# Kernel tuning notes

Hardware: AMD Instinct MI355X
Metric: run time of the kernel (lower is better)

The kernel has to match this reference:

```python
import jax, jax.numpy as jnp
import numpy as np

B, N, M = 2, 4096, 4096
QUERY_DIM, CONTEXT_DIM = 512, 768
H, D = 8, 64
INNER = H * D


def setup_inputs() -> dict:
    key = jax.random.key(0)
    ks = jax.random.split(key, 8)
    x = jax.random.normal(ks[0], (B, N, QUERY_DIM), dtype=jnp.float32)
    context_tensor = jax.random.normal(ks[1], (B, M, CONTEXT_DIM), dtype=jnp.float32)
    mask = jax.random.randint(ks[2], (B, M), 0, 2) > 0  # bool [B, M]
    s = 0.02
    Wq = jax.random.normal(ks[3], (QUERY_DIM, INNER), dtype=jnp.float32) * s
    Wk = jax.random.normal(ks[4], (CONTEXT_DIM, INNER), dtype=jnp.float32) * s
    Wv = jax.random.normal(ks[5], (CONTEXT_DIM, INNER), dtype=jnp.float32) * s
    Wo = jax.random.normal(ks[6], (INNER, QUERY_DIM), dtype=jnp.float32) * s
    bo = jnp.zeros((QUERY_DIM,), dtype=jnp.float32)
    return {"x": x, "context_tensor": context_tensor, "mask": mask,
            "Wq": Wq, "Wk": Wk, "Wv": Wv, "Wo": Wo, "bo": bo}


def reference(x, context_tensor, mask, Wq, Wk, Wv, Wo, bo):
    scale = D ** (-0.5)
    # projections -> [B, T, H, D]
    q = (x @ Wq).reshape(B, N, H, D)
    k = (context_tensor @ Wk).reshape(B, M, H, D)
    v = (context_tensor @ Wv).reshape(B, M, H, D)
    # scores [B, H, N, M]
    attn = jnp.einsum('bnhd,bmhd->bhnm', q, k) * scale
    neg = -jnp.finfo(attn.dtype).max
    attn = jnp.where(mask[:, None, None, :], attn, neg)
    attn = jax.nn.softmax(attn, axis=-1)
    out = jnp.einsum('bhnm,bmhd->bnhd', attn, v).reshape(B, N, INNER)
    return out @ Wo + bo  # dropout is 0.0 -> identity
```

## Files before the change

### kernel.cpp

```cpp
#include <hip/hip_runtime.h>

typedef unsigned short u16;
typedef unsigned int u32;
typedef __attribute__((ext_vector_type(8))) short bf16x8;
typedef __attribute__((ext_vector_type(4))) short bf16x4;
typedef __attribute__((ext_vector_type(4))) float f32x4;

#define CSC 0.1803368801111244f

__device__ __forceinline__ u16 f2b(float f) {
  union { float f; u32 u; } c; c.f = f;
  return (u16)((c.u + 0x8000u) >> 16);
}

__device__ __forceinline__ uint2 pk4(f32x4 p) {
  union { float f; u32 u; } c0, c1, c2, c3;
  c0.f = p[0]; c1.f = p[1]; c2.f = p[2]; c3.f = p[3];
  u32 a = c0.u + 0x8000u, b = c1.u + 0x8000u;
  u32 c = c2.u + 0x8000u, d = c3.u + 0x8000u;
  uint2 r;
  r.x = __builtin_amdgcn_perm(b, a, 0x07060302u);
  r.y = __builtin_amdgcn_perm(d, c, 0x07060302u);
  return r;
}

__device__ __forceinline__ bf16x4 pk4v(f32x4 p) {
  union { uint2 u; bf16x4 v; } c;
  c.u = pk4(p);
  return c.v;
}

__device__ __forceinline__ void async16(const void* g, void* s) {
  __builtin_amdgcn_global_load_lds(
      (const __attribute__((address_space(1))) u32*)g,
      (__attribute__((address_space(3))) u32*)s, 16, 0, 0);
}

__global__ void prep(const float* __restrict__ x, const float* __restrict__ ctx,
                     const int* __restrict__ mask,
                     const float* __restrict__ Wq, const float* __restrict__ Wk,
                     const float* __restrict__ Wv, const float* __restrict__ Wo,
                     u16* __restrict__ Xb, u16* __restrict__ Cb, float* __restrict__ mbf,
                     u16* __restrict__ Wtq, u16* __restrict__ Wtkv, u16* __restrict__ Wto) {
  __shared__ u16 Tl[64 * 65];
  const int bid = blockIdx.x, tid = threadIdx.x;
  if (bid < 10240) {
    const float* src; u16* dst; int i;
    if (bid < 4096) { i = (bid * 256 + tid) * 4; src = x; dst = Xb; }
    else { i = ((bid - 4096) * 256 + tid) * 4; src = ctx; dst = Cb; }
    float4 f = *(const float4*)&src[i];
    ushort4 o;
    o.x = f2b(f.x); o.y = f2b(f.y); o.z = f2b(f.z); o.w = f2b(f.w);
    *(ushort4*)&dst[i] = o;
  } else if (bid < 10560) {
    int t = bid - 10240;
    const float* W; u16* Wt; int Kd, tt;
    if (t < 64)       { W = Wq; Wt = Wtq;  Kd = 512; tt = t; }
    else if (t < 160) { W = Wk; Wt = Wtkv; Kd = 768; tt = t - 64; }
    else if (t < 256) { W = Wv; Wt = Wtkv + (size_t)512 * 768; Kd = 768; tt = t - 160; }
    else              { W = Wo; Wt = Wto;  Kd = 512; tt = t - 256; }
    const int k0 = (tt >> 3) * 64, n0 = (tt & 7) * 64;
    {
      const int r = tid >> 2, cg = (tid & 3) * 16;
#pragma unroll
      for (int i = 0; i < 4; i++) {
        float4 f = *(const float4*)&W[(size_t)(k0 + r) * 512 + n0 + cg + i * 4];
        Tl[r * 65 + cg + i * 4 + 0] = f2b(f.x);
        Tl[r * 65 + cg + i * 4 + 1] = f2b(f.y);
        Tl[r * 65 + cg + i * 4 + 2] = f2b(f.z);
        Tl[r * 65 + cg + i * 4 + 3] = f2b(f.w);
      }
    }
    __syncthreads();
    {
      const int n = tid >> 2, kg = (tid & 3) * 16;
      u16 buf[16];
#pragma unroll
      for (int i = 0; i < 16; i++) buf[i] = Tl[(kg + i) * 65 + n];
      u16* dst = &Wt[(size_t)(n0 + n) * Kd + k0 + kg];
      *(uint4*)dst = *(const uint4*)&buf[0];
      *(uint4*)(dst + 8) = *(const uint4*)&buf[8];
    }
  } else {
    int i = (bid - 10560) * 256 + tid;
    mbf[i] = mask[i] ? 0.f : -1e30f;
  }
}

__global__ __launch_bounds__(256, 2)
void gemm_qkv(const u16* __restrict__ Xb, const u16* __restrict__ Cb,
              const u16* __restrict__ Wtq, const u16* __restrict__ Wtkv,
              u16* __restrict__ Qb, u16* __restrict__ Kb, u16* __restrict__ Vt) {
  __shared__ u16 As[128 * 64];
  __shared__ u16 Bs[128 * 64];
  const int tid = threadIdx.x;
  const int w = tid >> 6, lane = tid & 63, quad = lane >> 4, l16 = lane & 15;
  const int wr = w >> 1, wc = w & 1;
  const int y = blockIdx.y;
  const bool isQ = (y < 4);
  const u16* A  = isQ ? Xb : Cb;
  const u16* Bt = isQ ? Wtq : Wtkv;
  const int K   = isQ ? 512 : 768;
  const int n0  = isQ ? y * 128 : (y - 4) * 128;
  const size_t m0 = (size_t)blockIdx.x * 128;
  const u16* Ab = A + m0 * K;
  const u16* Bb = Bt + (size_t)n0 * K;

  const int cswz = (((lane & 7) ^ ((lane >> 3) & 7)) << 3);
  const int sw0 = ((quad ^ (l16 & 7)) << 3);
  const int sw1 = sw0 ^ 32;
  const int rA = w * 32 + (lane >> 3);

  f32x4 acc[4][4];
#pragma unroll
  for (int i = 0; i < 4; i++)
#pragma unroll
    for (int j = 0; j < 4; j++) acc[i][j] = (f32x4){0.f, 0.f, 0.f, 0.f};

  for (int k0 = 0; k0 < K; k0 += 64) {
#pragma unroll
    for (int t = 0; t < 4; t++) {
      async16(Ab + (size_t)(rA + t * 8) * K + k0 + cswz, &As[(w * 32 + t * 8) * 64]);
      async16(Bb + (size_t)(rA + t * 8) * K + k0 + cswz, &Bs[(w * 32 + t * 8) * 64]);
    }
    __syncthreads();
#pragma unroll
    for (int ks = 0; ks < 2; ks++) {
      const int so = ks ? sw1 : sw0;
      bf16x8 af[4], bfr[4];
#pragma unroll
      for (int i = 0; i < 4; i++) {
        af[i]  = *(const bf16x8*)&As[(wr * 64 + i * 16 + l16) * 64 + so];
        bfr[i] = *(const bf16x8*)&Bs[(wc * 64 + i * 16 + l16) * 64 + so];
      }
#pragma unroll
      for (int i = 0; i < 4; i++)
#pragma unroll
        for (int j = 0; j < 4; j++)
          acc[i][j] = __builtin_amdgcn_mfma_f32_16x16x32_bf16(af[i], bfr[j], acc[i][j], 0, 0, 0);
    }
    __syncthreads();
  }

  if (!isQ && n0 >= 512) {
#pragma unroll
    for (int i = 0; i < 4; i++)
#pragma unroll
      for (int j = 0; j < 4; j++) {
        size_t row0 = m0 + wr * 64 + i * 16 + quad * 4;
        int d = n0 - 512 + wc * 64 + j * 16 + l16;
        *(uint2*)&Vt[(size_t)d * 8192 + row0] = pk4(acc[i][j]);
      }
  } else {
    u16* C0 = isQ ? Qb : Kb;
#pragma unroll
    for (int i = 0; i < 4; i++)
#pragma unroll
      for (int j = 0; j < 4; j++)
#pragma unroll
        for (int r = 0; r < 4; r++) {
          size_t row = m0 + wr * 64 + i * 16 + quad * 4 + r;
          int col = n0 + wc * 64 + j * 16 + l16;
          C0[row * 512 + col] = f2b(acc[i][j][r]);
        }
  }
}

__global__ __launch_bounds__(256, 2)
void gemm_o(const u16* __restrict__ A, const u16* __restrict__ Bt,
            const float* __restrict__ bias, float* __restrict__ Cf) {
  __shared__ u16 As[64 * 64];
  __shared__ u16 Bs[128 * 64];
  const int tid = threadIdx.x;
  const int w = tid >> 6, lane = tid & 63, quad = lane >> 4, l16 = lane & 15;
  const int wr = w >> 1, wc = w & 1;
  const size_t m0 = (size_t)blockIdx.x * 64;
  const int n0 = blockIdx.y * 128;
  const u16* Ab = A + m0 * 512;
  const u16* Bb = Bt + (size_t)n0 * 512;

  const int cswz = (((lane & 7) ^ ((lane >> 3) & 7)) << 3);
  const int sw0 = ((quad ^ (l16 & 7)) << 3);
  const int sw1 = sw0 ^ 32;
  const int r8 = lane >> 3;

  f32x4 acc[2][4];
#pragma unroll
  for (int i = 0; i < 2; i++)
#pragma unroll
    for (int j = 0; j < 4; j++) acc[i][j] = (f32x4){0.f, 0.f, 0.f, 0.f};

  for (int k0 = 0; k0 < 512; k0 += 64) {
#pragma unroll
    for (int t = 0; t < 2; t++)
      async16(Ab + (size_t)(w * 16 + t * 8 + r8) * 512 + k0 + cswz, &As[(w * 16 + t * 8) * 64]);
#pragma unroll
    for (int t = 0; t < 4; t++)
      async16(Bb + (size_t)(w * 32 + t * 8 + r8) * 512 + k0 + cswz, &Bs[(w * 32 + t * 8) * 64]);
    __syncthreads();
#pragma unroll
    for (int ks = 0; ks < 2; ks++) {
      const int so = ks ? sw1 : sw0;
      bf16x8 af[2], bfr[4];
#pragma unroll
      for (int i = 0; i < 2; i++)
        af[i] = *(const bf16x8*)&As[(wr * 32 + i * 16 + l16) * 64 + so];
#pragma unroll
      for (int j = 0; j < 4; j++)
        bfr[j] = *(const bf16x8*)&Bs[(wc * 64 + j * 16 + l16) * 64 + so];
#pragma unroll
      for (int i = 0; i < 2; i++)
#pragma unroll
        for (int j = 0; j < 4; j++)
          acc[i][j] = __builtin_amdgcn_mfma_f32_16x16x32_bf16(af[i], bfr[j], acc[i][j], 0, 0, 0);
    }
    __syncthreads();
  }

#pragma unroll
  for (int i = 0; i < 2; i++)
#pragma unroll
    for (int j = 0; j < 4; j++)
#pragma unroll
      for (int r = 0; r < 4; r++) {
        size_t row = m0 + wr * 32 + i * 16 + quad * 4 + r;
        int col = n0 + wc * 64 + j * 16 + l16;
        Cf[row * 512 + col] = acc[i][j][r] + bias[col];
      }
}

__global__ __launch_bounds__(256, 2)
void attn_kernel(const u16* __restrict__ Q, const u16* __restrict__ Kg,
                 const u16* __restrict__ Vt, const float* __restrict__ mbf,
                 u16* __restrict__ AO) {
  __shared__ u16 Ks[2][64 * 64];
  __shared__ u16 Vs[2][64 * 64];
  __shared__ float Mf[4096];

  const int tid = threadIdx.x;
  const int w = tid >> 6, lane = tid & 63, quad = lane >> 4, l16 = lane & 15;
  const int l = blockIdx.x;
  const int qb = l >> 4, hb = l & 15, h = hb >> 1, b = hb & 1;
  const size_t qrow0 = (size_t)b * 4096 + (size_t)qb * 128;
  const size_t crow0 = (size_t)b * 4096;
  const int hcol = h * 64;

  const int cswz = (((lane & 7) ^ ((lane >> 3) & 7)) << 3);
  const int sw0 = ((quad ^ (l16 & 7)) << 3);
  const int sw1 = sw0 ^ 32;
  const int r8 = lane >> 3;

  bf16x8 qf[2][2];
#pragma unroll
  for (int qt = 0; qt < 2; qt++)
#pragma unroll
    for (int ks = 0; ks < 2; ks++)
      qf[qt][ks] = *(const bf16x8*)&Q[(qrow0 + w * 32 + qt * 16 + l16) * 512 + hcol + ks * 32 + quad * 8];

  async16(Kg + (crow0 + w * 16 + r8) * 512 + hcol + cswz, &Ks[0][(w * 16) * 64]);
  async16(Kg + (crow0 + w * 16 + 8 + r8) * 512 + hcol + cswz, &Ks[0][(w * 16 + 8) * 64]);
  async16(Vt + (size_t)(hcol + w * 16 + r8) * 8192 + crow0 + cswz, &Vs[0][(w * 16) * 64]);
  async16(Vt + (size_t)(hcol + w * 16 + 8 + r8) * 8192 + crow0 + cswz, &Vs[0][(w * 16 + 8) * 64]);
#pragma unroll
  for (int t = 0; t < 4; t++) {
    int i = w * 4 + t;
    async16(mbf + crow0 + i * 256 + lane * 4, &Mf[i * 256]);
  }
  __syncthreads();

  f32x4 Oacc[2][4];
#pragma unroll
  for (int qt = 0; qt < 2; qt++)
#pragma unroll
    for (int dt = 0; dt < 4; dt++) Oacc[qt][dt] = (f32x4){0.f, 0.f, 0.f, 0.f};
  float lsum[2] = {0.f, 0.f};

  for (int mt = 0; mt < 64; mt++) {
    const int cur = mt & 1;
    const size_t m0 = (size_t)mt * 64;

    if (mt < 63) {
      const size_t mn = m0 + 64;
      async16(Kg + (crow0 + mn + w * 16 + r8) * 512 + hcol + cswz, &Ks[cur ^ 1][(w * 16) * 64]);
      async16(Kg + (crow0 + mn + w * 16 + 8 + r8) * 512 + hcol + cswz, &Ks[cur ^ 1][(w * 16 + 8) * 64]);
      async16(Vt + (size_t)(hcol + w * 16 + r8) * 8192 + crow0 + mn + cswz, &Vs[cur ^ 1][(w * 16) * 64]);
      async16(Vt + (size_t)(hcol + w * 16 + 8 + r8) * 8192 + crow0 + mn + cswz, &Vs[cur ^ 1][(w * 16 + 8) * 64]);
    }

    f32x4 mv[4];
#pragma unroll
    for (int mtt = 0; mtt < 4; mtt++)
      mv[mtt] = *(const f32x4*)&Mf[m0 + mtt * 16 + quad * 4];

    f32x4 sacc[2][4];
#pragma unroll
    for (int qt = 0; qt < 2; qt++)
#pragma unroll
      for (int mtt = 0; mtt < 4; mtt++) sacc[qt][mtt] = (f32x4){0.f, 0.f, 0.f, 0.f};
#pragma unroll
    for (int ks = 0; ks < 2; ks++) {
      const int so = ks ? sw1 : sw0;
      bf16x8 kb[4];
#pragma unroll
      for (int mtt = 0; mtt < 4; mtt++)
        kb[mtt] = *(const bf16x8*)&Ks[cur][(mtt * 16 + l16) * 64 + so];
#pragma unroll
      for (int qt = 0; qt < 2; qt++)
#pragma unroll
        for (int mtt = 0; mtt < 4; mtt++)
          sacc[qt][mtt] = __builtin_amdgcn_mfma_f32_16x16x32_bf16(kb[mtt], qf[qt][ks], sacc[qt][mtt], 0, 0, 0);
    }

    bf16x4 pf[2][4];
#pragma unroll
    for (int qt = 0; qt < 2; qt++) {
      float rs = 0.f;
#pragma unroll
      for (int mtt = 0; mtt < 4; mtt++) {
        f32x4 p;
#pragma unroll
        for (int r = 0; r < 4; r++) {
          p[r] = __builtin_amdgcn_exp2f(fmaf(sacc[qt][mtt][r], CSC, mv[mtt][r]));
          rs += p[r];
        }
        pf[qt][mtt] = pk4v(p);
      }
      lsum[qt] += rs;
    }

#pragma unroll
    for (int mtt = 0; mtt < 4; mtt++) {
      bf16x4 va[4];
#pragma unroll
      for (int dt = 0; dt < 4; dt++)
        va[dt] = *(const bf16x4*)&Vs[cur][(dt * 16 + l16) * 64 +
                    (((mtt * 2 + (quad >> 1)) ^ (l16 & 7)) << 3) + ((quad & 1) << 2)];
#pragma unroll
      for (int qt = 0; qt < 2; qt++)
#pragma unroll
        for (int dt = 0; dt < 4; dt++)
          Oacc[qt][dt] = __builtin_amdgcn_mfma_f32_16x16x16bf16_1k(va[dt], pf[qt][mtt], Oacc[qt][dt], 0, 0, 0);
    }
    __syncthreads();
  }

  float inv[2];
#pragma unroll
  for (int qt = 0; qt < 2; qt++) {
    float lv = lsum[qt];
    lv += __shfl_xor(lv, 16);
    lv += __shfl_xor(lv, 32);
    inv[qt] = 1.0f / lv;
  }

#pragma unroll
  for (int qt = 0; qt < 2; qt++)
#pragma unroll
    for (int dt = 0; dt < 4; dt++) {
      f32x4 o;
#pragma unroll
      for (int r = 0; r < 4; r++) o[r] = Oacc[qt][dt][r] * inv[qt];
      *(uint2*)&AO[(qrow0 + w * 32 + qt * 16 + l16) * 512 + hcol + dt * 16 + quad * 4] = pk4(o);
    }
}


extern "C" void kernel_launch(void* const* d_in, const int* in_sizes, int n_in,
                              void* d_out, int out_size, void* d_ws, size_t ws_size,
                              hipStream_t stream) {
  const float* x   = (const float*)d_in[0];
  const float* ctx = (const float*)d_in[1];
  const int*  mask = (const int*)d_in[2];
  const float* Wq  = (const float*)d_in[3];
  const float* Wk  = (const float*)d_in[4];
  const float* Wv  = (const float*)d_in[5];
  const float* Wo  = (const float*)d_in[6];
  const float* bo  = (const float*)d_in[7];
  float* out = (float*)d_out;

  char* p = (char*)d_ws;
  u16* Xb   = (u16*)p; p += (size_t)8192 * 512 * 2;
  u16* Cb   = (u16*)p; p += (size_t)8192 * 768 * 2;
  u16* Wtq  = (u16*)p; p += (size_t)512 * 512 * 2;
  u16* Wtkv = (u16*)p; p += (size_t)1024 * 768 * 2;
  u16* Wto  = (u16*)p; p += (size_t)512 * 512 * 2;
  u16* Qb   = (u16*)p; p += (size_t)8192 * 512 * 2;
  u16* Kb   = (u16*)p; p += (size_t)8192 * 512 * 2;
  u16* Vtg  = (u16*)p; p += (size_t)512 * 8192 * 2;
  u16* AOb  = (u16*)p; p += (size_t)8192 * 512 * 2;
  float* mbf = (float*)p; p += (size_t)8192 * 4;

  prep<<<10592, 256, 0, stream>>>(x, ctx, mask, Wq, Wk, Wv, Wo,
                                  Xb, Cb, mbf, Wtq, Wtkv, Wto);
  gemm_qkv<<<dim3(64, 12), 256, 0, stream>>>(Xb, Cb, Wtq, Wtkv, Qb, Kb, Vtg);
  attn_kernel<<<512, 256, 0, stream>>>(Qb, Kb, Vtg, mbf, AOb);
  gemm_o<<<dim3(128, 4), 256, 0, stream>>>(AOb, Wto, bo, out);
}
```

Before: 240.9 us.

## Fold key mask and softmax scale into K/V projections and shrink tiles

The projection GEMM now multiplies K rows by the mask and the softmax scale, and multiplies V rows by the mask. Masked keys therefore give a zero score, so exp2 yields exactly 1 and a zero V contribution. The attention kernel drops the per-tile mask loads and the FMA before exp2, then corrects the row sum by subtracting the per-batch count of masked keys, which prep computes. All three GEMM and attention kernels move to smaller tiles (64-row blocks), with more blocks and higher launch-bound occupancy targets. The trade-off is less K/V reuse per attention block and more global traffic in exchange for more parallelism and fewer instructions per tile.

```diff
diff --git a/kernel.cpp b/kernel.cpp
--- a/kernel.cpp
+++ b/kernel.cpp
@@ -40,9 +40,11 @@
                      const int* __restrict__ mask,
                      const float* __restrict__ Wq, const float* __restrict__ Wk,
                      const float* __restrict__ Wv, const float* __restrict__ Wo,
-                     u16* __restrict__ Xb, u16* __restrict__ Cb, float* __restrict__ mbf,
+                     u16* __restrict__ Xb, u16* __restrict__ Cb,
+                     float* __restrict__ mvalid, float* __restrict__ cnt,
                      u16* __restrict__ Wtq, u16* __restrict__ Wtkv, u16* __restrict__ Wto) {
   __shared__ u16 Tl[64 * 65];
+  __shared__ int cred[4];
   const int bid = blockIdx.x, tid = threadIdx.x;
   if (bid < 10240) {
     const float* src; u16* dst; int i;
@@ -82,16 +84,31 @@
       *(uint4*)(dst + 8) = *(const uint4*)&buf[8];
     }
   } else {
-    int i = (bid - 10560) * 256 + tid;
-    mbf[i] = mask[i] ? 0.f : -1e30f;
-  }
-}
-
-__global__ __launch_bounds__(256, 2)
+    const int b = bid - 10560;
+    const int base = b * 4096;
+    const int w = tid >> 6, lane = tid & 63;
+    int zc = 0;
+#pragma unroll
+    for (int j = 0; j < 16; j++) {
+      int idx = tid + j * 256;
+      int mv = mask[base + idx];
+      mvalid[base + idx] = mv ? 1.f : 0.f;
+      zc += (mv == 0);
+    }
+#pragma unroll
+    for (int d = 1; d < 64; d <<= 1) zc += __shfl_xor(zc, d);
+    if (lane == 0) cred[w] = zc;
+    __syncthreads();
+    if (tid == 0) cnt[b] = (float)(cred[0] + cred[1] + cred[2] + cred[3]);
+  }
+}
+
+__global__ __launch_bounds__(256, 6)
 void gemm_qkv(const u16* __restrict__ Xb, const u16* __restrict__ Cb,
               const u16* __restrict__ Wtq, const u16* __restrict__ Wtkv,
+              const float* __restrict__ mvalid,
               u16* __restrict__ Qb, u16* __restrict__ Kb, u16* __restrict__ Vt) {
-  __shared__ u16 As[128 * 64];
+  __shared__ u16 As[64 * 64];
   __shared__ u16 Bs[128 * 64];
   const int tid = threadIdx.x;
   const int w = tid >> 6, lane = tid & 63, quad = lane >> 4, l16 = lane & 15;
@@ -102,82 +119,9 @@
   const u16* Bt = isQ ? Wtq : Wtkv;
   const int K   = isQ ? 512 : 768;
   const int n0  = isQ ? y * 128 : (y - 4) * 128;
-  const size_t m0 = (size_t)blockIdx.x * 128;
+  const size_t m0 = (size_t)blockIdx.x * 64;
   const u16* Ab = A + m0 * K;
   const u16* Bb = Bt + (size_t)n0 * K;
-
-  const int cswz = (((lane & 7) ^ ((lane >> 3) & 7)) << 3);
-  const int sw0 = ((quad ^ (l16 & 7)) << 3);
-  const int sw1 = sw0 ^ 32;
-  const int rA = w * 32 + (lane >> 3);
-
-  f32x4 acc[4][4];
-#pragma unroll
-  for (int i = 0; i < 4; i++)
-#pragma unroll
-    for (int j = 0; j < 4; j++) acc[i][j] = (f32x4){0.f, 0.f, 0.f, 0.f};
-
-  for (int k0 = 0; k0 < K; k0 += 64) {
-#pragma unroll
-    for (int t = 0; t < 4; t++) {
-      async16(Ab + (size_t)(rA + t * 8) * K + k0 + cswz, &As[(w * 32 + t * 8) * 64]);
-      async16(Bb + (size_t)(rA + t * 8) * K + k0 + cswz, &Bs[(w * 32 + t * 8) * 64]);
-    }
-    __syncthreads();
-#pragma unroll
-    for (int ks = 0; ks < 2; ks++) {
-      const int so = ks ? sw1 : sw0;
-      bf16x8 af[4], bfr[4];
-#pragma unroll
-      for (int i = 0; i < 4; i++) {
-        af[i]  = *(const bf16x8*)&As[(wr * 64 + i * 16 + l16) * 64 + so];
-        bfr[i] = *(const bf16x8*)&Bs[(wc * 64 + i * 16 + l16) * 64 + so];
-      }
-#pragma unroll
-      for (int i = 0; i < 4; i++)
-#pragma unroll
-        for (int j = 0; j < 4; j++)
-          acc[i][j] = __builtin_amdgcn_mfma_f32_16x16x32_bf16(af[i], bfr[j], acc[i][j], 0, 0, 0);
-    }
-    __syncthreads();
-  }
-
-  if (!isQ && n0 >= 512) {
-#pragma unroll
-    for (int i = 0; i < 4; i++)
-#pragma unroll
-      for (int j = 0; j < 4; j++) {
-        size_t row0 = m0 + wr * 64 + i * 16 + quad * 4;
-        int d = n0 - 512 + wc * 64 + j * 16 + l16;
-        *(uint2*)&Vt[(size_t)d * 8192 + row0] = pk4(acc[i][j]);
-      }
-  } else {
-    u16* C0 = isQ ? Qb : Kb;
-#pragma unroll
-    for (int i = 0; i < 4; i++)
-#pragma unroll
-      for (int j = 0; j < 4; j++)
-#pragma unroll
-        for (int r = 0; r < 4; r++) {
-          size_t row = m0 + wr * 64 + i * 16 + quad * 4 + r;
-          int col = n0 + wc * 64 + j * 16 + l16;
-          C0[row * 512 + col] = f2b(acc[i][j][r]);
-        }
-  }
-}
-
-__global__ __launch_bounds__(256, 2)
-void gemm_o(const u16* __restrict__ A, const u16* __restrict__ Bt,
-            const float* __restrict__ bias, float* __restrict__ Cf) {
-  __shared__ u16 As[64 * 64];
-  __shared__ u16 Bs[128 * 64];
-  const int tid = threadIdx.x;
-  const int w = tid >> 6, lane = tid & 63, quad = lane >> 4, l16 = lane & 15;
-  const int wr = w >> 1, wc = w & 1;
-  const size_t m0 = (size_t)blockIdx.x * 64;
-  const int n0 = blockIdx.y * 128;
-  const u16* Ab = A + m0 * 512;
-  const u16* Bb = Bt + (size_t)n0 * 512;
 
   const int cswz = (((lane & 7) ^ ((lane >> 3) & 7)) << 3);
   const int sw0 = ((quad ^ (l16 & 7)) << 3);
@@ -190,13 +134,12 @@
 #pragma unroll
     for (int j = 0; j < 4; j++) acc[i][j] = (f32x4){0.f, 0.f, 0.f, 0.f};
 
-  for (int k0 = 0; k0 < 512; k0 += 64) {
-#pragma unroll
-    for (int t = 0; t < 2; t++)
-      async16(Ab + (size_t)(w * 16 + t * 8 + r8) * 512 + k0 + cswz, &As[(w * 16 + t * 8) * 64]);
+  for (int k0 = 0; k0 < K; k0 += 64) {
+    async16(Ab + (size_t)(w * 16 + r8) * K + k0 + cswz, &As[(w * 16) * 64]);
+    async16(Ab + (size_t)(w * 16 + 8 + r8) * K + k0 + cswz, &As[(w * 16 + 8) * 64]);
 #pragma unroll
     for (int t = 0; t < 4; t++)
-      async16(Bb + (size_t)(w * 32 + t * 8 + r8) * 512 + k0 + cswz, &Bs[(w * 32 + t * 8) * 64]);
+      async16(Bb + (size_t)(w * 32 + t * 8 + r8) * K + k0 + cswz, &Bs[(w * 32 + t * 8) * 64]);
     __syncthreads();
 #pragma unroll
     for (int ks = 0; ks < 2; ks++) {
@@ -217,63 +160,130 @@
     __syncthreads();
   }
 
-#pragma unroll
-  for (int i = 0; i < 2; i++)
-#pragma unroll
-    for (int j = 0; j < 4; j++)
-#pragma unroll
-      for (int r = 0; r < 4; r++) {
-        size_t row = m0 + wr * 32 + i * 16 + quad * 4 + r;
-        int col = n0 + wc * 64 + j * 16 + l16;
-        Cf[row * 512 + col] = acc[i][j][r] + bias[col];
-      }
-}
-
-__global__ __launch_bounds__(256, 2)
+  if (isQ) {
+#pragma unroll
+    for (int i = 0; i < 2; i++)
+#pragma unroll
+      for (int j = 0; j < 4; j++)
+#pragma unroll
+        for (int r = 0; r < 4; r++) {
+          size_t row = m0 + wr * 32 + i * 16 + quad * 4 + r;
+          Qb[row * 512 + n0 + wc * 64 + j * 16 + l16] = f2b(acc[i][j][r]);
+        }
+  } else if (n0 < 512) {
+#pragma unroll
+    for (int i = 0; i < 2; i++) {
+      size_t row0 = m0 + wr * 32 + i * 16 + quad * 4;
+      f32x4 vm = *(const f32x4*)&mvalid[row0];
+#pragma unroll
+      for (int j = 0; j < 4; j++)
+#pragma unroll
+        for (int r = 0; r < 4; r++)
+          Kb[(row0 + r) * 512 + n0 + wc * 64 + j * 16 + l16] = f2b(acc[i][j][r] * (vm[r] * CSC));
+    }
+  } else {
+#pragma unroll
+    for (int i = 0; i < 2; i++) {
+      size_t row0 = m0 + wr * 32 + i * 16 + quad * 4;
+      f32x4 vm = *(const f32x4*)&mvalid[row0];
+#pragma unroll
+      for (int j = 0; j < 4; j++) {
+        int d = n0 - 512 + wc * 64 + j * 16 + l16;
+        f32x4 v;
+#pragma unroll
+        for (int r = 0; r < 4; r++) v[r] = acc[i][j][r] * vm[r];
+        *(uint2*)&Vt[(size_t)d * 8192 + row0] = pk4(v);
+      }
+    }
+  }
+}
+
+__global__ __launch_bounds__(256, 4)
+void gemm_o(const u16* __restrict__ A, const u16* __restrict__ Bt,
+            const float* __restrict__ bias, float* __restrict__ Cf) {
+  __shared__ u16 As[64 * 64];
+  __shared__ u16 Bs[64 * 64];
+  const int tid = threadIdx.x;
+  const int w = tid >> 6, lane = tid & 63, quad = lane >> 4, l16 = lane & 15;
+  const size_t m0 = (size_t)blockIdx.x * 64;
+  const int n0 = blockIdx.y * 64;
+  const u16* Ab = A + m0 * 512;
+  const u16* Bb = Bt + (size_t)n0 * 512;
+
+  const int cswz = (((lane & 7) ^ ((lane >> 3) & 7)) << 3);
+  const int sw0 = ((quad ^ (l16 & 7)) << 3);
+  const int sw1 = sw0 ^ 32;
+  const int r8 = lane >> 3;
+
+  f32x4 acc[4];
+#pragma unroll
+  for (int j = 0; j < 4; j++) acc[j] = (f32x4){0.f, 0.f, 0.f, 0.f};
+
+  for (int k0 = 0; k0 < 512; k0 += 64) {
+    async16(Ab + (size_t)(w * 16 + r8) * 512 + k0 + cswz, &As[(w * 16) * 64]);
+    async16(Ab + (size_t)(w * 16 + 8 + r8) * 512 + k0 + cswz, &As[(w * 16 + 8) * 64]);
+    async16(Bb + (size_t)(w * 16 + r8) * 512 + k0 + cswz, &Bs[(w * 16) * 64]);
+    async16(Bb + (size_t)(w * 16 + 8 + r8) * 512 + k0 + cswz, &Bs[(w * 16 + 8) * 64]);
+    __syncthreads();
+#pragma unroll
+    for (int ks = 0; ks < 2; ks++) {
+      const int so = ks ? sw1 : sw0;
+      bf16x8 af = *(const bf16x8*)&As[(w * 16 + l16) * 64 + so];
+#pragma unroll
+      for (int j = 0; j < 4; j++) {
+        bf16x8 bfr = *(const bf16x8*)&Bs[(j * 16 + l16) * 64 + so];
+        acc[j] = __builtin_amdgcn_mfma_f32_16x16x32_bf16(af, bfr, acc[j], 0, 0, 0);
+      }
+    }
+    __syncthreads();
+  }
+
+#pragma unroll
+  for (int j = 0; j < 4; j++)
+#pragma unroll
+    for (int r = 0; r < 4; r++) {
+      size_t row = m0 + w * 16 + quad * 4 + r;
+      int col = n0 + j * 16 + l16;
+      Cf[row * 512 + col] = acc[j][r] + bias[col];
+    }
+}
+
+__global__ __launch_bounds__(256, 4)
 void attn_kernel(const u16* __restrict__ Q, const u16* __restrict__ Kg,
-                 const u16* __restrict__ Vt, const float* __restrict__ mbf,
+                 const u16* __restrict__ Vt, const float* __restrict__ cnt,
                  u16* __restrict__ AO) {
   __shared__ u16 Ks[2][64 * 64];
   __shared__ u16 Vs[2][64 * 64];
-  __shared__ float Mf[4096];
 
   const int tid = threadIdx.x;
   const int w = tid >> 6, lane = tid & 63, quad = lane >> 4, l16 = lane & 15;
   const int l = blockIdx.x;
   const int qb = l >> 4, hb = l & 15, h = hb >> 1, b = hb & 1;
-  const size_t qrow0 = (size_t)b * 4096 + (size_t)qb * 128;
+  const size_t qrow0 = (size_t)b * 4096 + (size_t)qb * 64;
   const size_t crow0 = (size_t)b * 4096;
   const int hcol = h * 64;
+  const float cb = cnt[b];
 
   const int cswz = (((lane & 7) ^ ((lane >> 3) & 7)) << 3);
   const int sw0 = ((quad ^ (l16 & 7)) << 3);
   const int sw1 = sw0 ^ 32;
   const int r8 = lane >> 3;
 
-  bf16x8 qf[2][2];
-#pragma unroll
-  for (int qt = 0; qt < 2; qt++)
-#pragma unroll
-    for (int ks = 0; ks < 2; ks++)
-      qf[qt][ks] = *(const bf16x8*)&Q[(qrow0 + w * 32 + qt * 16 + l16) * 512 + hcol + ks * 32 + quad * 8];
+  bf16x8 qf[2];
+#pragma unroll
+  for (int ks = 0; ks < 2; ks++)
+    qf[ks] = *(const bf16x8*)&Q[(qrow0 + w * 16 + l16) * 512 + hcol + ks * 32 + quad * 8];
 
   async16(Kg + (crow0 + w * 16 + r8) * 512 + hcol + cswz, &Ks[0][(w * 16) * 64]);
   async16(Kg + (crow0 + w * 16 + 8 + r8) * 512 + hcol + cswz, &Ks[0][(w * 16 + 8) * 64]);
   async16(Vt + (size_t)(hcol + w * 16 + r8) * 8192 + crow0 + cswz, &Vs[0][(w * 16) * 64]);
   async16(Vt + (size_t)(hcol + w * 16 + 8 + r8) * 8192 + crow0 + cswz, &Vs[0][(w * 16 + 8) * 64]);
-#pragma unroll
-  for (int t = 0; t < 4; t++) {
-    int i = w * 4 + t;
-    async16(mbf + crow0 + i * 256 + lane * 4, &Mf[i * 256]);
-  }
   __syncthreads();
 
-  f32x4 Oacc[2][4];
-#pragma unroll
-  for (int qt = 0; qt < 2; qt++)
-#pragma unroll
-    for (int dt = 0; dt < 4; dt++) Oacc[qt][dt] = (f32x4){0.f, 0.f, 0.f, 0.f};
-  float lsum[2] = {0.f, 0.f};
+  f32x4 Oacc[4];
+#pragma unroll
+  for (int dt = 0; dt < 4; dt++) Oacc[dt] = (f32x4){0.f, 0.f, 0.f, 0.f};
+  float lsum = 0.f;
 
   for (int mt = 0; mt < 64; mt++) {
     const int cur = mt & 1;
@@ -287,81 +297,54 @@
       async16(Vt + (size_t)(hcol + w * 16 + 8 + r8) * 8192 + crow0 + mn + cswz, &Vs[cur ^ 1][(w * 16 + 8) * 64]);
     }
 
-    f32x4 mv[4];
-#pragma unroll
-    for (int mtt = 0; mtt < 4; mtt++)
-      mv[mtt] = *(const f32x4*)&Mf[m0 + mtt * 16 + quad * 4];
-
-    f32x4 sacc[2][4];
-#pragma unroll
-    for (int qt = 0; qt < 2; qt++)
-#pragma unroll
-      for (int mtt = 0; mtt < 4; mtt++) sacc[qt][mtt] = (f32x4){0.f, 0.f, 0.f, 0.f};
+    f32x4 sacc[4];
+#pragma unroll
+    for (int mtt = 0; mtt < 4; mtt++) sacc[mtt] = (f32x4){0.f, 0.f, 0.f, 0.f};
 #pragma unroll
     for (int ks = 0; ks < 2; ks++) {
       const int so = ks ? sw1 : sw0;
-      bf16x8 kb[4];
-#pragma unroll
-      for (int mtt = 0; mtt < 4; mtt++)
-        kb[mtt] = *(const bf16x8*)&Ks[cur][(mtt * 16 + l16) * 64 + so];
-#pragma unroll
-      for (int qt = 0; qt < 2; qt++)
-#pragma unroll
-        for (int mtt = 0; mtt < 4; mtt++)
-          sacc[qt][mtt] = __builtin_amdgcn_mfma_f32_16x16x32_bf16(kb[mtt], qf[qt][ks], sacc[qt][mtt], 0, 0, 0);
-    }
-
-    bf16x4 pf[2][4];
-#pragma unroll
-    for (int qt = 0; qt < 2; qt++) {
-      float rs = 0.f;
 #pragma unroll
       for (int mtt = 0; mtt < 4; mtt++) {
-        f32x4 p;
-#pragma unroll
-        for (int r = 0; r < 4; r++) {
-          p[r] = __builtin_amdgcn_exp2f(fmaf(sacc[qt][mtt][r], CSC, mv[mtt][r]));
-          rs += p[r];
-        }
-        pf[qt][mtt] = pk4v(p);
-      }
-      lsum[qt] += rs;
-    }
-
+        bf16x8 kb = *(const bf16x8*)&Ks[cur][(mtt * 16 + l16) * 64 + so];
+        sacc[mtt] = __builtin_amdgcn_mfma_f32_16x16x32_bf16(kb, qf[ks], sacc[mtt], 0, 0, 0);
+      }
+    }
+
+    bf16x4 pf[4];
 #pragma unroll
     for (int mtt = 0; mtt < 4; mtt++) {
-      bf16x4 va[4];
-#pragma unroll
-      for (int dt = 0; dt < 4; dt++)
-        va[dt] = *(const bf16x4*)&Vs[cur][(dt * 16 + l16) * 64 +
-                    (((mtt * 2 + (quad >> 1)) ^ (l16 & 7)) << 3) + ((quad & 1) << 2)];
-#pragma unroll
-      for (int qt = 0; qt < 2; qt++)
-#pragma unroll
-        for (int dt = 0; dt < 4; dt++)
-          Oacc[qt][dt] = __builtin_amdgcn_mfma_f32_16x16x16bf16_1k(va[dt], pf[qt][mtt], Oacc[qt][dt], 0, 0, 0);
-    }
-    __syncthreads();
-  }
-
-  float inv[2];
-#pragma unroll
-  for (int qt = 0; qt < 2; qt++) {
-    float lv = lsum[qt];
-    lv += __shfl_xor(lv, 16);
-    lv += __shfl_xor(lv, 32);
-    inv[qt] = 1.0f / lv;
-  }
-
-#pragma unroll
-  for (int qt = 0; qt < 2; qt++)
-#pragma unroll
-    for (int dt = 0; dt < 4; dt++) {
-      f32x4 o;
-#pragma unroll
-      for (int r = 0; r < 4; r++) o[r] = Oacc[qt][dt][r] * inv[qt];
-      *(uint2*)&AO[(qrow0 + w * 32 + qt * 16 + l16) * 512 + hcol + dt * 16 + quad * 4] = pk4(o);
-    }
+      f32x4 p;
+#pragma unroll
+      for (int r = 0; r < 4; r++) {
+        p[r] = __builtin_amdgcn_exp2f(sacc[mtt][r]);
+        lsum += p[r];
+      }
+      pf[mtt] = pk4v(p);
+    }
+
+#pragma unroll
+    for (int mtt = 0; mtt < 4; mtt++) {
+#pragma unroll
+      for (int dt = 0; dt < 4; dt++) {
+        bf16x4 va = *(const bf16x4*)&Vs[cur][(dt * 16 + l16) * 64 +
+                      (((mtt * 2 + (quad >> 1)) ^ (l16 & 7)) << 3) + ((quad & 1) << 2)];
+        Oacc[dt] = __builtin_amdgcn_mfma_f32_16x16x16bf16_1k(va, pf[mtt], Oacc[dt], 0, 0, 0);
+      }
+    }
+    __syncthreads();
+  }
+
+  lsum += __shfl_xor(lsum, 16);
+  lsum += __shfl_xor(lsum, 32);
+  const float inv = 1.0f / (lsum - cb);
+
+#pragma unroll
+  for (int dt = 0; dt < 4; dt++) {
+    f32x4 o;
+#pragma unroll
+    for (int r = 0; r < 4; r++) o[r] = Oacc[dt][r] * inv;
+    *(uint2*)&AO[(qrow0 + w * 16 + l16) * 512 + hcol + dt * 16 + quad * 4] = pk4(o);
+  }
 }
 
 
@@ -388,11 +371,12 @@
   u16* Kb   = (u16*)p; p += (size_t)8192 * 512 * 2;
   u16* Vtg  = (u16*)p; p += (size_t)512 * 8192 * 2;
   u16* AOb  = (u16*)p; p += (size_t)8192 * 512 * 2;
-  float* mbf = (float*)p; p += (size_t)8192 * 4;
-
-  prep<<<10592, 256, 0, stream>>>(x, ctx, mask, Wq, Wk, Wv, Wo,
-                                  Xb, Cb, mbf, Wtq, Wtkv, Wto);
-  gemm_qkv<<<dim3(64, 12), 256, 0, stream>>>(Xb, Cb, Wtq, Wtkv, Qb, Kb, Vtg);
-  attn_kernel<<<512, 256, 0, stream>>>(Qb, Kb, Vtg, mbf, AOb);
-  gemm_o<<<dim3(128, 4), 256, 0, stream>>>(AOb, Wto, bo, out);
-}
+  float* mvalid = (float*)p; p += (size_t)8192 * 4;
+  float* cnt    = (float*)p; p += 2 * 4;
+
+  prep<<<10562, 256, 0, stream>>>(x, ctx, mask, Wq, Wk, Wv, Wo,
+                                  Xb, Cb, mvalid, cnt, Wtq, Wtkv, Wto);
+  gemm_qkv<<<dim3(128, 12), 256, 0, stream>>>(Xb, Cb, Wtq, Wtkv, mvalid, Qb, Kb, Vtg);
+  attn_kernel<<<1024, 256, 0, stream>>>(Qb, Kb, Vtg, cnt, AOb);
+  gemm_o<<<dim3(128, 8), 256, 0, stream>>>(AOb, Wto, bo, out);
+}
```

After: 226.3 us. -6.0%, faster.
